# Optimization experiments

Hardware: AMD Instinct MI355X
Metric: run time of the kernel (lower is better)

The kernel has to match this reference:

```python
import jax, jax.numpy as jnp
import numpy as np

N = 100800          # anchors for YOLOv5 @ 1280px: 3*(160^2+80^2+40^2)
NC = 80             # COCO classes
CONF_THRES = 0.4
IOU_THRES = 0.45
MAX_DET = 1000
MAX_NMS = 4096      # candidate cap before IoU (ultralytics uses 30000; reduced for KxK IoU memory)
MAX_WH = 7680.0     # per-class box offset (agnostic=False)


def setup_inputs() -> dict:
    key = jax.random.key(0)
    k1, k2, k3, k4 = jax.random.split(key, 4)
    xy = jax.random.uniform(k1, (1, N, 2), jnp.float32) * 1280.0   # box centers
    wh = jax.random.uniform(k2, (1, N, 2), jnp.float32) * 200.0 + 2.0  # box sizes
    obj = jax.random.uniform(k3, (1, N, 1), jnp.float32)           # objectness
    cls = jax.random.uniform(k4, (1, N, NC), jnp.float32)          # class scores
    pred = jnp.concatenate([xy, wh, obj, cls], axis=-1)            # [1, N, 85]
    return {"pred": pred}


def _xywh2xyxy(b):
    xy, wh = b[:, :2], b[:, 2:4]
    return jnp.concatenate([xy - wh * 0.5, xy + wh * 0.5], axis=-1)


def _nms(pred):
    p = pred[0]                                   # [N, 85] (module returns image 0)
    cls_conf = p[:, 5:] * p[:, 4:5]               # conf = obj * cls
    conf = jnp.max(cls_conf, axis=-1)             # best-class confidence [N]
    cls = jnp.argmax(cls_conf, axis=-1)           # best-class index [N]
    box = _xywh2xyxy(p[:, :4])                    # [N, 4] xyxy

    # candidate filter (conf > thres) + cap to top MAX_NMS by confidence
    scores = jnp.where(conf > CONF_THRES, conf, -jnp.inf)
    top_s, idx = jax.lax.top_k(scores, MAX_NMS)   # sorted descending
    b = box[idx]                                  # [K, 4]
    c = cls[idx]                                  # [K]
    valid = top_s > CONF_THRES                    # [K]

    # per-class NMS: offset boxes by class index so classes never overlap
    ob = b + (c.astype(b.dtype) * MAX_WH)[:, None]
    area = (ob[:, 2] - ob[:, 0]) * (ob[:, 3] - ob[:, 1])
    lt = jnp.maximum(ob[:, None, :2], ob[None, :, :2])
    rb = jnp.minimum(ob[:, None, 2:], ob[None, :, 2:])
    whi = jnp.clip(rb - lt, 0.0)
    inter = whi[..., 0] * whi[..., 1]             # [K, K]
    iou = inter / (area[:, None] + area[None, :] - inter + 1e-9)

    # greedy NMS: box j is suppressed if a kept, higher-scoring box i overlaps it
    upper = jnp.triu(jnp.ones((MAX_NMS, MAX_NMS), bool), 1)
    sup_mat = jax.lax.stop_gradient((iou > IOU_THRES) & upper)

    def body(i, keep):
        return keep & ~(sup_mat[i] & keep[i])

    keep = jax.lax.stop_gradient(jax.lax.fori_loop(0, MAX_NMS, body, valid))

    # top max_det kept detections, padded with zeros -> fixed [MAX_DET, 6]
    fscore = jnp.where(keep, top_s, -jnp.inf)
    fs, fi = jax.lax.top_k(fscore, MAX_DET)
    out = jnp.concatenate(
        [b[fi], top_s[fi][:, None], c[fi].astype(b.dtype)[:, None]], axis=-1
    )                                             # [MAX_DET, 6] = x1,y1,x2,y2,conf,cls
    return jnp.where((fs > CONF_THRES)[:, None], out, 0.0)


def reference(pred):
    return _nms(pred)
```

## Files before the change

kernel.cpp:

```cpp
#include <hip/hip_runtime.h>
#include <stdint.h>

#pragma clang fp contract(off)

#define N_ANCH 100800
#define ROWLEN 85
#define NCLS 80
#define CONF_T 0.4f
#define IOU_T 0.45f
#define MAXNMS 4096
#define MAXDET 1000
#define NBINS 4096
#define MAX_WH_F 7680.0f
#define SROWS 128
#define SCORE_BLKS ((N_ANCH + SROWS - 1) / SROWS)


__device__ __forceinline__ unsigned long long aload64(const unsigned long long* p) {
  return __hip_atomic_load(p, __ATOMIC_RELAXED, __HIP_MEMORY_SCOPE_AGENT);
}
__device__ __forceinline__ void astore64(unsigned long long* p, unsigned long long v) {
  __hip_atomic_store(p, v, __ATOMIC_RELAXED, __HIP_MEMORY_SCOPE_AGENT);
}
__device__ __forceinline__ unsigned aload32(const unsigned* p) {
  return __hip_atomic_load(p, __ATOMIC_RELAXED, __HIP_MEMORY_SCOPE_AGENT);
}
__device__ __forceinline__ void astore32(unsigned* p, unsigned v) {
  __hip_atomic_store(p, v, __ATOMIC_RELAXED, __HIP_MEMORY_SCOPE_AGENT);
}

__global__ __launch_bounds__(256) void score_kernel(
    const float* __restrict__ pred, float* __restrict__ confArr,
    unsigned char* __restrict__ clsArr, unsigned short* __restrict__ binArr,
    unsigned* __restrict__ hist, unsigned* __restrict__ base,
    unsigned* __restrict__ meta) {
  __shared__ float s[SROWS * ROWLEN];
  __shared__ unsigned s_scan[4];
  __shared__ unsigned s_last;
  const int tid = threadIdx.x;
  const int wid = tid >> 6, lane = tid & 63;

  {
    const float4* p4 = (const float4*)pred;
    float4* s4 = (float4*)s;
    const int NV = SROWS * ROWLEN / 4;
    const size_t g0 = (size_t)blockIdx.x * NV;
    const size_t gmax = (size_t)N_ANCH * ROWLEN / 4;
    for (int v = tid; v < NV; v += 256) {
      size_t g = g0 + v;
      if (g < gmax) s4[v] = p4[g];
    }
  }
  __syncthreads();

  if (tid < SROWS) {
    int n = blockIdx.x * SROWS + tid;
    if (n < N_ANCH) {
      const float* row = s + tid * ROWLEN;
      float obj = row[4];
      float best = row[5] * obj;
      int bc = 0;
      for (int i = 1; i < NCLS; ++i) {
        float v = row[5 + i] * obj;
        if (v > best) { best = v; bc = i; }
      }
      confArr[n] = best;
      clsArr[n] = (unsigned char)bc;
      unsigned short bo = 0;
      if (best > CONF_T) {
        int b = (int)(best * 4096.0f);
        if (b > NBINS - 1) b = NBINS - 1;
        bo = (unsigned short)b;
        atomicAdd(&hist[b], 1u);
      }
      binArr[n] = bo;
    }
  }

  __syncthreads();
  if (tid == 0) {
    unsigned ret = __hip_atomic_fetch_add(&meta[8], 1u, __ATOMIC_RELAXED,
                                          __HIP_MEMORY_SCOPE_AGENT);
    s_last = (ret == (unsigned)(SCORE_BLKS - 1)) ? 1u : 0u;
  }
  __syncthreads();
  if (s_last == 0) return;

  unsigned hv[16];
  unsigned ssum = 0;
#pragma unroll
  for (int k = 0; k < 16; ++k) {
    hv[k] = aload32(&hist[NBINS - 1 - (tid * 16 + k)]);
    ssum += hv[k];
  }
  unsigned incl = ssum;
  for (int d = 1; d < 64; d <<= 1) {
    unsigned v = __shfl_up(incl, d);
    if (lane >= d) incl += v;
  }
  if (lane == 63) s_scan[wid] = incl;
  __syncthreads();
  if (tid == 0) {
    unsigned acc = 0;
    for (int w = 0; w < 4; ++w) { unsigned t = s_scan[w]; s_scan[w] = acc; acc += t; }
  }
  __syncthreads();
  unsigned e = s_scan[wid] + (incl - ssum);
#pragma unroll
  for (int k = 0; k < 16; ++k) {
    int b = NBINS - 1 - (tid * 16 + k);
    base[b] = e;
    if (e <= (unsigned)MAXNMS && e + hv[k] > (unsigned)MAXNMS) {
      meta[0] = (unsigned)(b + 1);
      meta[1] = e;
    }
    e += hv[k];
  }
  if (tid == 255) meta[2] = e;
}

__global__ __launch_bounds__(256) void tail_kernel(
    const float* __restrict__ pred, const float* __restrict__ confArr,
    const unsigned char* __restrict__ clsArr,
    const unsigned short* __restrict__ binArr,
    const unsigned* __restrict__ base, unsigned* __restrict__ cnt,
    unsigned* __restrict__ meta, unsigned long long* __restrict__ cand,
    unsigned* __restrict__ keep32, unsigned long long* __restrict__ sortedKey,
    float* __restrict__ out) {
  __shared__ unsigned long long s_cand[MAXNMS];
  __shared__ unsigned long long s_mkey[128];
  __shared__ unsigned s_mslot[128];
  __shared__ float4 s_obox[128];
  __shared__ unsigned long long s_okey[128];
  __shared__ unsigned s_oslot[128];
  __shared__ unsigned s_K;
  __shared__ unsigned s_scan[4];
  __shared__ unsigned s_last;
  __shared__ unsigned short s_kept[MAXDET];
  __shared__ unsigned s_tot;

  const int tid = threadIdx.x;
  const int wid = tid >> 6, lane = tid & 63;
  const int c = blockIdx.x;

  const unsigned Bcut = meta[0];
  const unsigned total =
      Bcut ? meta[1] : (meta[2] > (unsigned)MAXNMS ? (unsigned)MAXNMS : meta[2]);

  {
    const int gtid = c * 256 + tid;
    for (int v = gtid; v < N_ANCH / 4; v += NCLS * 256) {
      ushort4 b4 = ((const ushort4*)binArr)[v];
      int n0 = v * 4;
#pragma unroll
      for (int k = 0; k < 4; ++k) {
        unsigned b = (k == 0) ? b4.x : (k == 1) ? b4.y : (k == 2) ? b4.z : b4.w;
        if (b && b >= Bcut) {
          int n = n0 + k;
          unsigned r = atomicAdd(&cnt[b], 1u);
          astore64(&cand[base[b] + r],
                   ((unsigned long long)__float_as_uint(confArr[n]) << 32) |
                       (unsigned long long)(~(unsigned)n));
        }
      }
    }
  }

  __syncthreads();
  if (tid == 0) {
    __hip_atomic_fetch_add(&meta[10], 1u, __ATOMIC_RELAXED,
                           __HIP_MEMORY_SCOPE_AGENT);
    while (aload32(&meta[10]) < (unsigned)NCLS) __builtin_amdgcn_s_sleep(2);
  }
  __syncthreads();

  if (tid == 0) s_K = 0;
  for (int i = tid; i < MAXNMS; i += 256)
    s_cand[i] = (i < (int)total) ? aload64(&cand[i]) : 0ull;
  __syncthreads();

  for (int i = tid; i < (int)total; i += 256) {
    unsigned long long key = s_cand[i];
    unsigned a = ~(unsigned)key;
    if (clsArr[a] == (unsigned char)c) {
      float conf = __uint_as_float((unsigned)(key >> 32));
      int b = (int)(conf * 4096.0f);
      if (b > NBINS - 1) b = NBINS - 1;
      unsigned bs = base[b], ct = aload32(&cnt[b]);
      unsigned r = 0;
      for (unsigned j = 0; j < ct; ++j) r += (s_cand[bs + j] > key) ? 1u : 0u;
      unsigned slot = bs + r;
      unsigned idx = atomicAdd(&s_K, 1u);
      if (idx < 128) { s_mkey[idx] = key; s_mslot[idx] = slot; }
    }
  }
  __syncthreads();
  int K = (int)s_K;
  if (K > 128) K = 128;
  if (K > 0) {
    if (tid < K) {
      unsigned myslot = s_mslot[tid];
      unsigned ord = 0;
      for (int j = 0; j < K; ++j) ord += (s_mslot[j] < myslot) ? 1u : 0u;
      unsigned long long key = s_mkey[tid];
      unsigned a = ~(unsigned)key;
      const float* row = pred + (size_t)a * ROWLEN;
      float bx = row[0], by = row[1], bw = row[2], bh = row[3];
      float x1 = bx - bw * 0.5f, y1 = by - bh * 0.5f;
      float x2 = bx + bw * 0.5f, y2 = by + bh * 0.5f;
      float off = (float)c * MAX_WH_F;
      s_obox[ord] = make_float4(x1 + off, y1 + off, x2 + off, y2 + off);
      s_okey[ord] = key;
      s_oslot[ord] = myslot;
    }
    __syncthreads();
    if (wid == 0) {
      const int nch = (K + 63) >> 6;
      float ox1[2], oy1[2], ox2[2], oy2[2];
#pragma unroll
      for (int q = 0; q < 2; ++q) {
        ox1[q] = oy1[q] = ox2[q] = oy2[q] = 0.f;
        int j = q * 64 + lane;
        if (q < nch && j < K) {
          float4 bb = s_obox[j];
          ox1[q] = bb.x; oy1[q] = bb.y; ox2[q] = bb.z; oy2[q] = bb.w;
        }
      }
      unsigned long long cm00 = 0ull, cm01 = 0ull, cm10 = 0ull, cm11 = 0ull;
#pragma unroll
      for (int qi = 0; qi < 2; ++qi) {
        if (qi < nch) {
          int lim = K - qi * 64; if (lim > 64) lim = 64;
          for (int li = 0; li < lim; ++li) {
            float bx1 = __shfl(qi ? ox1[1] : ox1[0], li);
            float by1 = __shfl(qi ? oy1[1] : oy1[0], li);
            float bx2 = __shfl(qi ? ox2[1] : ox2[0], li);
            float by2 = __shfl(qi ? oy2[1] : oy2[0], li);
            float areai = (bx2 - bx1) * (by2 - by1);
            int i = qi * 64 + li;
            unsigned long long bit = (1ull << li);
#pragma unroll
            for (int q = 0; q < 2; ++q) {
              if (q < nch) {
                int j = q * 64 + lane;
                float ltx = fmaxf(bx1, ox1[q]);
                float lty = fmaxf(by1, oy1[q]);
                float rbx = fminf(bx2, ox2[q]);
                float rby = fminf(by2, oy2[q]);
                float iw = fmaxf(rbx - ltx, 0.f);
                float ih = fmaxf(rby - lty, 0.f);
                float inter = iw * ih;
                float areaj = (ox2[q] - ox1[q]) * (oy2[q] - oy1[q]);
                float iou = inter / (areai + areaj - inter + 1e-9f);
                bool sup = (iou > IOU_T) && (i < j) && (j < K);
                if (sup) {
                  if (q == 0) { if (qi == 0) cm00 |= bit; else cm01 |= bit; }
                  else       { if (qi == 0) cm10 |= bit; else cm11 |= bit; }
                }
              }
            }
          }
        }
      }
      unsigned long long vm0, vm1, km0, km1;
      {
        int r0 = K;      vm0 = (r0 >= 64) ? ~0ull : ((1ull << r0) - 1ull);
        int r1 = K - 64; vm1 = (r1 >= 64) ? ~0ull
                                          : ((r1 <= 0) ? 0ull : ((1ull << r1) - 1ull));
        km0 = vm0; km1 = vm1;
      }
      for (int it = 0; it < 200; ++it) {
        unsigned long long s0 = cm00 & km0;
        if (nch > 1) s0 |= cm01 & km1;
        unsigned long long b0 = __ballot(s0 == 0ull) & vm0;
        unsigned long long b1 = km1;
        if (nch > 1) {
          unsigned long long s1 = (cm10 & km0) | (cm11 & km1);
          b1 = __ballot(s1 == 0ull) & vm1;
        }
        bool same = (b0 == km0) && (b1 == km1);
        km0 = b0; km1 = b1;
        if (same) break;
      }
#pragma unroll
      for (int q = 0; q < 2; ++q) {
        int j = q * 64 + lane;
        if (q < nch && j < K) {
          unsigned slot = s_oslot[j];
          astore32(&keep32[slot],
                   (unsigned)(((q == 0 ? km0 : km1) >> lane) & 1ull));
          astore64(&sortedKey[slot], s_okey[j]);
        }
      }
    }
  }

  __syncthreads();
  if (tid == 0) {
    unsigned ret = __hip_atomic_fetch_add(&meta[9], 1u, __ATOMIC_RELAXED,
                                          __HIP_MEMORY_SCOPE_AGENT);
    s_last = (ret == (unsigned)(NCLS - 1)) ? 1u : 0u;
  }
  __syncthreads();
  if (s_last == 0) return;

  unsigned flags[16];
  unsigned fsum = 0;
#pragma unroll
  for (int k = 0; k < 16; ++k) {
    flags[k] = aload32(&keep32[tid * 16 + k]);
    fsum += flags[k];
  }
  unsigned incl = fsum;
  for (int d = 1; d < 64; d <<= 1) {
    unsigned v = __shfl_up(incl, d);
    if (lane >= d) incl += v;
  }
  if (lane == 63) s_scan[wid] = incl;
  __syncthreads();
  if (tid == 0) {
    unsigned acc = 0;
    for (int w = 0; w < 4; ++w) { unsigned t = s_scan[w]; s_scan[w] = acc; acc += t; }
    s_tot = acc;
  }
  __syncthreads();
  unsigned rank = s_scan[wid] + (incl - fsum);
#pragma unroll
  for (int k = 0; k < 16; ++k) {
    if (flags[k]) {
      if (rank < MAXDET) s_kept[rank] = (unsigned short)(tid * 16 + k);
      rank++;
    }
  }
  __syncthreads();
  unsigned tot = s_tot;
  for (int r = tid; r < MAXDET; r += 256) {
    float* o = out + (size_t)r * 6;
    if (r < (int)tot) {
      int slot = s_kept[r];
      unsigned long long key = aload64(&sortedKey[slot]);
      unsigned a = ~(unsigned)key;
      float conf = __uint_as_float((unsigned)(key >> 32));
      const float* row = pred + (size_t)a * ROWLEN;
      float bx = row[0], by = row[1], bw = row[2], bh = row[3];
      o[0] = bx - bw * 0.5f; o[1] = by - bh * 0.5f;
      o[2] = bx + bw * 0.5f; o[3] = by + bh * 0.5f;
      o[4] = conf; o[5] = (float)clsArr[a];
    } else {
      o[0] = 0.f; o[1] = 0.f; o[2] = 0.f;
      o[3] = 0.f; o[4] = 0.f; o[5] = 0.f;
    }
  }
}

extern "C" void kernel_launch(void* const* d_in, const int* in_sizes, int n_in,
                              void* d_out, int out_size, void* d_ws, size_t ws_size,
                              hipStream_t stream) {
  (void)in_sizes; (void)n_in; (void)out_size; (void)ws_size;
  const float* pred = (const float*)d_in[0];
  float* out = (float*)d_out;
  char* ws = (char*)d_ws;

  unsigned* hist = (unsigned*)(ws + 0);
  unsigned* cnt = (unsigned*)(ws + 16384);
  unsigned* keep32 = (unsigned*)(ws + 32768);
  unsigned* meta = (unsigned*)(ws + 49152);
  unsigned* base = (unsigned*)(ws + 49280);
  unsigned long long* cand = (unsigned long long*)(ws + 65664);
  unsigned long long* sortedKey = (unsigned long long*)(ws + 98432);
  float* confArr = (float*)(ws + 131200);
  unsigned char* clsArr = (unsigned char*)(ws + 534400);
  unsigned short* binArr = (unsigned short*)(ws + 635200);

  hipMemsetAsync(ws, 0, 49280, stream);

  score_kernel<<<SCORE_BLKS, 256, 0, stream>>>(pred, confArr, clsArr, binArr,
                                               hist, base, meta);
  tail_kernel<<<NCLS, 256, 0, stream>>>(pred, confArr, clsArr, binArr, base,
                                        cnt, meta, cand, keep32, sortedKey, out);
}
```

Baseline: 141.0 us.

## Split candidate gather into its own kernel, replacing in-kernel grid barrier

Result: faster. 133.8 us (-5.1%).

```diff
diff --git a/kernel.cpp b/kernel.cpp
--- a/kernel.cpp
+++ b/kernel.cpp
@@ -119,12 +119,32 @@
   if (tid == 255) meta[2] = e;
 }
 
-__global__ __launch_bounds__(256) void tail_kernel(
-    const float* __restrict__ pred, const float* __restrict__ confArr,
-    const unsigned char* __restrict__ clsArr,
-    const unsigned short* __restrict__ binArr,
+__global__ __launch_bounds__(256) void gather_kernel(
+    const float* __restrict__ confArr, const unsigned short* __restrict__ binArr,
     const unsigned* __restrict__ base, unsigned* __restrict__ cnt,
-    unsigned* __restrict__ meta, unsigned long long* __restrict__ cand,
+    const unsigned* __restrict__ meta, unsigned long long* __restrict__ cand) {
+  int v = blockIdx.x * 256 + threadIdx.x;
+  if (v >= N_ANCH / 4) return;
+  ushort4 b4 = ((const ushort4*)binArr)[v];
+  const unsigned Bcut = meta[0];
+  int n0 = v * 4;
+#pragma unroll
+  for (int k = 0; k < 4; ++k) {
+    unsigned b = (k == 0) ? b4.x : (k == 1) ? b4.y : (k == 2) ? b4.z : b4.w;
+    if (b && b >= Bcut) {
+      int n = n0 + k;
+      unsigned r = atomicAdd(&cnt[b], 1u);
+      cand[base[b] + r] =
+          ((unsigned long long)__float_as_uint(confArr[n]) << 32) |
+          (unsigned long long)(~(unsigned)n);
+    }
+  }
+}
+
+__global__ __launch_bounds__(256) void class_kernel(
+    const float* __restrict__ pred, const unsigned char* __restrict__ clsArr,
+    const unsigned* __restrict__ base, const unsigned* __restrict__ cnt,
+    unsigned* __restrict__ meta, const unsigned long long* __restrict__ cand,
     unsigned* __restrict__ keep32, unsigned long long* __restrict__ sortedKey,
     float* __restrict__ out) {
   __shared__ unsigned long long s_cand[MAXNMS];
@@ -147,36 +167,16 @@
   const unsigned total =
       Bcut ? meta[1] : (meta[2] > (unsigned)MAXNMS ? (unsigned)MAXNMS : meta[2]);
 
+  if (tid == 0) s_K = 0;
   {
-    const int gtid = c * 256 + tid;
-    for (int v = gtid; v < N_ANCH / 4; v += NCLS * 256) {
-      ushort4 b4 = ((const ushort4*)binArr)[v];
-      int n0 = v * 4;
-#pragma unroll
-      for (int k = 0; k < 4; ++k) {
-        unsigned b = (k == 0) ? b4.x : (k == 1) ? b4.y : (k == 2) ? b4.z : b4.w;
-        if (b && b >= Bcut) {
-          int n = n0 + k;
-          unsigned r = atomicAdd(&cnt[b], 1u);
-          astore64(&cand[base[b] + r],
-                   ((unsigned long long)__float_as_uint(confArr[n]) << 32) |
-                       (unsigned long long)(~(unsigned)n));
-        }
-      }
-    }
-  }
-
-  __syncthreads();
-  if (tid == 0) {
-    __hip_atomic_fetch_add(&meta[10], 1u, __ATOMIC_RELAXED,
-                           __HIP_MEMORY_SCOPE_AGENT);
-    while (aload32(&meta[10]) < (unsigned)NCLS) __builtin_amdgcn_s_sleep(2);
-  }
-  __syncthreads();
-
-  if (tid == 0) s_K = 0;
-  for (int i = tid; i < MAXNMS; i += 256)
-    s_cand[i] = (i < (int)total) ? aload64(&cand[i]) : 0ull;
+    const ulonglong2* c2 = (const ulonglong2*)cand;
+    for (int v = tid; v < MAXNMS / 2; v += 256) {
+      ulonglong2 kk = c2[v];
+      int i0 = v * 2, i1 = i0 + 1;
+      s_cand[i0] = (i0 < (int)total) ? kk.x : 0ull;
+      s_cand[i1] = (i1 < (int)total) ? kk.y : 0ull;
+    }
+  }
   __syncthreads();
 
   for (int i = tid; i < (int)total; i += 256) {
@@ -186,7 +186,7 @@
       float conf = __uint_as_float((unsigned)(key >> 32));
       int b = (int)(conf * 4096.0f);
       if (b > NBINS - 1) b = NBINS - 1;
-      unsigned bs = base[b], ct = aload32(&cnt[b]);
+      unsigned bs = base[b], ct = cnt[b];
       unsigned r = 0;
       for (unsigned j = 0; j < ct; ++j) r += (s_cand[bs + j] > key) ? 1u : 0u;
       unsigned slot = bs + r;
@@ -376,6 +376,8 @@
 
   score_kernel<<<SCORE_BLKS, 256, 0, stream>>>(pred, confArr, clsArr, binArr,
                                                hist, base, meta);
-  tail_kernel<<<NCLS, 256, 0, stream>>>(pred, confArr, clsArr, binArr, base,
-                                        cnt, meta, cand, keep32, sortedKey, out);
-}
+  gather_kernel<<<(N_ANCH / 4 + 255) / 256, 256, 0, stream>>>(
+      confArr, binArr, base, cnt, meta, cand);
+  class_kernel<<<NCLS, 256, 0, stream>>>(pred, clsArr, base, cnt, meta, cand,
+                                         keep32, sortedKey, out);
+}
```
